# Performance work log

Measured on AMD Instinct MI355X. Metric: run time of the kernel, lower is better.

Reference implementation:

```python
import jax, jax.numpy as jnp
import numpy as np

POI, EMB, UNITS, QDIM, B = 5000, 256, 512, 256, 64


def setup_inputs() -> dict:
    key = jax.random.key(0)
    ks = jax.random.split(key, 16)
    s = 0.05
    return {
        "x": jax.random.randint(ks[0], (B,), 0, POI),
        "query": jax.random.normal(ks[1], (B, QDIM), jnp.float32),
        "poi_embedding": jax.random.normal(ks[2], (POI, EMB), jnp.float32),
        "A_hat": jax.random.normal(ks[3], (B, B), jnp.float32),
        "dec_hidden": jax.random.normal(ks[4], (B, UNITS), jnp.float32),
        "cat_dec_hidden": jax.random.normal(ks[5], (1, B, UNITS), jnp.float32),
        # GRUCell params (keras order z, r, h; reset_after=True -> bias [2, 3*units])
        "gru_kernel": jax.random.normal(ks[6], (EMB + QDIM, 3 * UNITS), jnp.float32) * s,
        "gru_rec_kernel": jax.random.normal(ks[7], (UNITS, 3 * UNITS), jnp.float32) * s,
        "gru_bias": jax.random.normal(ks[8], (2, 3 * UNITS), jnp.float32) * s,
        # Bahdanau attention params
        "W1_w": jax.random.normal(ks[9], (EMB, UNITS), jnp.float32) * s,
        "W1_b": jnp.zeros((UNITS,), jnp.float32),
        "W2_w": jax.random.normal(ks[10], (UNITS, UNITS), jnp.float32) * s,
        "W2_b": jnp.zeros((UNITS,), jnp.float32),
        "V_w": jax.random.normal(ks[11], (UNITS, 1), jnp.float32) * s,
        "V_b": jnp.zeros((1,), jnp.float32),
        # output dense: concat(context EMB, output_ UNITS, cat_hidden UNITS) -> POI
        "fc_w": jax.random.normal(ks[12], (EMB + 2 * UNITS, POI), jnp.float32) * s,
        "fc_b": jnp.zeros((POI,), jnp.float32),
    }


def _gru_cell(x, h, kernel, rec_kernel, bias):
    # keras GRUCell, reset_after=True, gate order (z, r, h)
    xm = x @ kernel + bias[0]        # [B, 3U]
    hm = h @ rec_kernel + bias[1]    # [B, 3U]
    xz, xr, xh = jnp.split(xm, 3, axis=-1)
    hz, hr, hh = jnp.split(hm, 3, axis=-1)
    z = jax.nn.sigmoid(xz + hz)
    r = jax.nn.sigmoid(xr + hr)
    h_cand = jnp.tanh(xh + r * hh)
    h_new = z * h + (1.0 - z) * h_cand
    return h_new, h_new


def reference(x, query, poi_embedding, A_hat, dec_hidden, cat_dec_hidden,
              gru_kernel, gru_rec_kernel, gru_bias,
              W1_w, W1_b, W2_w, W2_b, V_w, V_b, fc_w, fc_b):
    emb = poi_embedding
    x1 = jnp.concatenate([emb[x], query], axis=1)          # [B, EMB+QDIM]
    output_, state = _gru_cell(x1, dec_hidden, gru_kernel, gru_rec_kernel, gru_bias)
    # Bahdanau attention: values are the full embedding table [POI, EMB]
    v_proj = emb @ W1_w + W1_b                              # [POI, U]
    q_proj = output_ @ W2_w + W2_b                          # [B, U]
    score = jnp.tanh(v_proj[None, :, :] + q_proj[:, None, :]) @ V_w + V_b  # [B, POI, 1]
    attn = jax.nn.softmax(score, axis=1)                    # [B, POI, 1]
    context = jnp.sum(attn * emb[None, :, :], axis=1)       # [B, EMB]
    out_cat = jnp.concatenate([context, output_, cat_dec_hidden[0]], axis=1)
    logits = out_cat @ fc_w + fc_b                          # [B, POI]
    return (logits, state, output_)
```

## Files before the change

kernel.cpp:

```cpp
#include <hip/hip_runtime.h>
#include <hip/hip_bf16.h>

typedef __bf16 bf16;
typedef __bf16 bf16x8 __attribute__((ext_vector_type(8)));
typedef float f32x4 __attribute__((ext_vector_type(4)));

#define BB 64
#define EMB 256
#define UNITS 512
#define POI 5000
#define KCAT 1280
#define SCLD 5024
#define L2E 1.4426950408889634f

__device__ __forceinline__ float rcp_(float x){ return __builtin_amdgcn_rcpf(x); }
__device__ __forceinline__ float exp2_(float x){ return __builtin_amdgcn_exp2f(x); }

__device__ __forceinline__ f32x4 mm16r(const float* __restrict__ ap, const float* __restrict__ B,
                                       int ldb, int K, int nc, int lane){
  int q = lane >> 4;
  f32x4 acc = {0.f,0.f,0.f,0.f};
  ap += q*8;
  const float* bp = B + (size_t)(q*8)*ldb + nc;
#pragma unroll 2
  for(int k0 = 0; k0 < K; k0 += 32){
    f32x4 a0 = *(const f32x4*)ap;
    f32x4 a1 = *(const f32x4*)(ap+4);
    bf16x8 a, b;
#pragma unroll
    for(int j=0;j<4;j++){ a[j] = (bf16)a0[j]; a[4+j] = (bf16)a1[j]; }
#pragma unroll
    for(int j=0;j<8;j++) b[j] = (bf16)bp[(size_t)j*ldb];
    acc = __builtin_amdgcn_mfma_f32_16x16x32_bf16(a, b, acc, 0, 0, 0);
    ap += 32; bp += (size_t)32*ldb;
  }
  return acc;
}

__device__ __forceinline__ f32x4 mm16f(const float* __restrict__ A, const float* __restrict__ B,
                                       int lda, int ldb, int K, int mr, int nc, int lane){
  return mm16r(A + (size_t)mr*lda, B, ldb, K, nc, lane);
}

__global__ __launch_bounds__(256) void k_prep0(const float* __restrict__ W1,
    float* __restrict__ W1T, float* __restrict__ out){
  int t = blockIdx.x*256 + threadIdx.x;
  for(int i=t; i<BB*POI; i+=32768) out[i] = 0.f;
  for(int i=t; i<EMB*UNITS; i+=32768){
    int r = i >> 9, c = i & 511;
    W1T[(size_t)c*EMB + r] = W1[i];
  }
}

__global__ __launch_bounds__(256) void k_gru(const int* __restrict__ x, const float* __restrict__ query,
    const float* __restrict__ emb, const float* __restrict__ h0,
    const float* __restrict__ gruK, const float* __restrict__ gruR,
    float* __restrict__ xmP, float* __restrict__ hmP){
  int lane = threadIdx.x & 63, w = threadIdx.x >> 6;
  int col = blockIdx.x*16 + (lane & 15);
  int z = blockIdx.z;
  int mr = w*16 + (lane & 15);
  const float* arow;
  const float* B;
  float* C;
  if(blockIdx.y){
    arow = h0 + (size_t)mr*512 + z*256;
    B = gruR + (size_t)(z*256)*1536;
    C = hmP + (size_t)z*BB*1536;
  } else {
    arow = z ? (query + (size_t)mr*256) : (emb + (size_t)x[mr]*EMB);
    B = gruK + (size_t)(z*256)*1536;
    C = xmP + (size_t)z*BB*1536;
  }
  f32x4 acc = mm16r(arow, B, 1536, 256, col, lane);
  int rb = w*16 + (lane >> 4)*4;
#pragma unroll
  for(int r=0;r<4;r++) C[(size_t)(rb+r)*1536 + col] = acc[r];
}

__global__ void k_gates(const float* __restrict__ xmP, const float* __restrict__ hmP,
                        const float* __restrict__ bias, const float* __restrict__ h0,
                        const float* __restrict__ catd,
                        float* __restrict__ hn, float* __restrict__ outc, float* __restrict__ dout){
  int b = blockIdx.x, u = threadIdx.x;
  const float* x0 = xmP + b*1536; const float* x1s = xmP + (size_t)BB*1536 + b*1536;
  const float* h0s = hmP + b*1536; const float* h1s = hmP + (size_t)BB*1536 + b*1536;
  float xz = x0[u]      + x1s[u]      + bias[u];
  float xg = x0[512+u]  + x1s[512+u]  + bias[512+u];
  float xh = x0[1024+u] + x1s[1024+u] + bias[1024+u];
  float hz = h0s[u]      + h1s[u]      + bias[1536+u];
  float hg = h0s[512+u]  + h1s[512+u]  + bias[2048+u];
  float hh = h0s[1024+u] + h1s[1024+u] + bias[2560+u];
  float z = rcp_(1.f + exp2_(-L2E*(xz+hz)));
  float r = rcp_(1.f + exp2_(-L2E*(xg+hg)));
  float ca = xh + r*hh;
  ca = fminf(fmaxf(ca, -15.f), 15.f);
  float e = exp2_(2.f*L2E*ca);
  float hc = (e - 1.f)*rcp_(e + 1.f);
  float h = h0[b*512+u];
  float v = z*h + (1.f - z)*hc;
  hn[b*512+u] = v;
  outc[b*KCAT + 256 + u] = v;
  outc[b*KCAT + 768 + u] = catd[(size_t)b*512 + u];
  dout[(size_t)POI*BB + (size_t)b*512 + u] = v;
  dout[(size_t)POI*BB + (size_t)BB*512 + (size_t)b*512 + u] = v;
}

__global__ __launch_bounds__(256) void k_qproj(const float* __restrict__ hn, const float* __restrict__ W2,
                        const float* __restrict__ W2b, float* __restrict__ Eq){
  int lane = threadIdx.x & 63, w = threadIdx.x >> 6;
  int col = blockIdx.x*16 + (lane & 15);
  f32x4 acc = mm16f(hn, W2, UNITS, UNITS, UNITS, w*16 + (lane & 15), col, lane);
  float bn = W2b[col];
  int rb = w*16 + (lane >> 4)*4;
#pragma unroll
  for(int r=0;r<4;r++){
    float v = (acc[r] + bn)*(2.f*L2E);
    Eq[(rb+r)*UNITS + col] = exp2_(fminf(fmaxf(v, -40.f), 40.f));
  }
}

template<int NY>
__global__ __launch_bounds__(256, 4) void k_vscore(
    const float* __restrict__ emb, const float* __restrict__ W1T,
    const float* __restrict__ W1b, const float* __restrict__ Eq,
    const float* __restrict__ Vw, float* __restrict__ scS){
  constexpr int USL = 512/NY;
  __shared__ float evsT[USL][36];
  __shared__ float qs[64][USL+4];
  __shared__ float vws[USL];
  int t = threadIdx.x, lane = t & 63, w = t >> 6;
  int p0 = blockIdx.x*32, uh = blockIdx.y*USL;
  int q = lane >> 4;
#pragma unroll
  for(int i=0;i<USL/64;i++){
    int colL = (w + 4*i)*16 + (lane & 15);
    float bn = W1b[uh + colL];
    const float* brow = W1T + (size_t)(uh+colL)*EMB + q*8;
#pragma unroll
    for(int pq=0;pq<2;pq++){
      int mr = p0 + pq*16 + (lane & 15); if(mr >= POI) mr = POI-1;
      const float* ap = emb + (size_t)mr*EMB + q*8;
      const float* bp = brow;
      f32x4 acc = {0.f,0.f,0.f,0.f};
#pragma unroll 2
      for(int k0=0;k0<EMB;k0+=32){
        f32x4 a0 = *(const f32x4*)ap, a1 = *(const f32x4*)(ap+4);
        f32x4 b0 = *(const f32x4*)bp, b1 = *(const f32x4*)(bp+4);
        bf16x8 a, b;
#pragma unroll
        for(int j=0;j<4;j++){ a[j]=(bf16)a0[j]; a[4+j]=(bf16)a1[j];
                              b[j]=(bf16)b0[j]; b[4+j]=(bf16)b1[j]; }
        acc = __builtin_amdgcn_mfma_f32_16x16x32_bf16(a,b,acc,0,0,0);
        ap += 32; bp += 32;
      }
      f32x4 ev;
#pragma unroll
      for(int r=0;r<4;r++){
        float v = (acc[r] + bn)*(2.f*L2E);
        ev[r] = exp2_(fminf(fmaxf(v,-40.f),40.f));
      }
      *(f32x4*)&evsT[colL][pq*16 + q*4] = ev;
    }
  }
  constexpr int CG = USL/4;
  for(int i=t; i<64*CG; i+=256){
    int b = i/CG, cg = i - b*CG;
    *(f32x4*)&qs[b][cg*4] = *(const f32x4*)&Eq[b*UNITS + uh + cg*4];
  }
  if(t < USL) vws[t] = Vw[uh + t];
  __syncthreads();
  int pg = t & 7, bg = t >> 3;
  const float* q0r = &qs[2*bg][0];
  const float* q1r = &qs[2*bg+1][0];
  f32x4 s0 = {0.f,0.f,0.f,0.f}, s1 = {0.f,0.f,0.f,0.f};
#pragma unroll 2
  for(int u4=0; u4<USL/4; ++u4){
    f32x4 q0 = *(const f32x4*)&q0r[u4*4];
    f32x4 q1 = *(const f32x4*)&q1r[u4*4];
    f32x4 wv = *(const f32x4*)&vws[u4*4];
#pragma unroll
    for(int j=0;j<4;j++){
      f32x4 ev = *(const f32x4*)&evsT[u4*4+j][4*pg];
#pragma unroll
      for(int e=0;e<4;e++){
        s0[e] += wv[j]*rcp_(ev[e]*q0[j] + 1.f);
        s1[e] += wv[j]*rcp_(ev[e]*q1[j] + 1.f);
      }
    }
  }
  float* srow = scS + (size_t)blockIdx.y*BB*SCLD + (size_t)(2*bg)*SCLD + p0 + 4*pg;
  int pA = p0 + 4*pg;
  if(pA + 3 < POI){
    *(f32x4*)srow = s0;
    *(f32x4*)(srow + SCLD) = s1;
  } else {
#pragma unroll
    for(int e=0;e<4;e++) if(pA+e < POI){ srow[e] = s0[e]; srow[SCLD+e] = s1[e]; }
  }
}

__global__ __launch_bounds__(512) void k_softmax(float* __restrict__ sc, const float* __restrict__ Vw,
                                                 float* __restrict__ outc, float* __restrict__ ivb,
                                                 int nslab){
  __shared__ float red[512];
  int b = blockIdx.x, t = threadIdx.x;
  if(t < 256) outc[b*KCAT + t] = 0.f;
  red[t] = Vw[t];
  __syncthreads();
  for(int o=256;o>0;o>>=1){ if(t<o) red[t]+=red[t+o]; __syncthreads(); }
  float SW = red[0]; __syncthreads();
  float* sA = sc + (size_t)b*SCLD;
  float mx = -3.4e38f;
  for(int p=t;p<POI;p+=512){
    float acc = sA[p];
    for(int y=1;y<nslab;y++) acc += sA[(size_t)y*BB*SCLD + p];
    float s = SW - 2.f*acc;
    sA[p] = s;
    mx = fmaxf(mx, s);
  }
  red[t] = mx; __syncthreads();
  for(int o=256;o>0;o>>=1){ if(t<o) red[t]=fmaxf(red[t],red[t+o]); __syncthreads(); }
  float M = red[0]; __syncthreads();
  float sum = 0.f;
  for(int p=t;p<POI;p+=512){
    float wv = exp2_((sA[p] - M)*L2E);
    sA[p] = wv;
    sum += wv;
  }
  red[t] = sum; __syncthreads();
  for(int o=256;o>0;o>>=1){ if(t<o) red[t]+=red[t+o]; __syncthreads(); }
  if(t == 0) ivb[b] = rcp_(red[0]);
  if(t < SCLD-POI) sA[POI + t] = 0.f;
}

__global__ __launch_bounds__(256) void k_ctx(const float* __restrict__ wb, const float* __restrict__ emb,
                                             const float* __restrict__ ivb, float* __restrict__ outc){
  int lane = threadIdx.x & 63, w = threadIdx.x >> 6;
  int n = blockIdx.x*16 + (lane & 15);
  int ky = blockIdx.y;
  int kbeg = ky*384;
  int mr = w*16 + (lane & 15);
  f32x4 acc = mm16f(wb + kbeg, emb + (size_t)kbeg*EMB, SCLD, EMB, 384, mr, n, lane);
  if(ky == 12){
    int q = lane >> 4;
    const float* ap = wb + (size_t)mr*SCLD + 4992 + q*8;
    bf16x8 a, bfr;
#pragma unroll
    for(int j=0;j<8;j++) a[j] = (bf16)ap[j];
#pragma unroll
    for(int j=0;j<8;j++){
      int k = 4992 + q*8 + j; int kc = k < POI ? k : POI-1;
      bfr[j] = (bf16)emb[(size_t)kc*EMB + n];
    }
    acc = __builtin_amdgcn_mfma_f32_16x16x32_bf16(a, bfr, acc, 0, 0, 0);
  }
  int rb = w*16 + (lane >> 4)*4;
#pragma unroll
  for(int r=0;r<4;r++) atomicAdd(&outc[(size_t)(rb+r)*KCAT + n], acc[r]*ivb[rb+r]);
}

__global__ __launch_bounds__(256) void k_logits(const float* __restrict__ A, const float* __restrict__ Bw,
                        const float* __restrict__ fcb, float* __restrict__ out){
  int lane = threadIdx.x & 63, w = threadIdx.x >> 6;
  int n = blockIdx.x*16 + (lane & 15);
  int nc = n < POI ? n : POI-1;
  int ky = blockIdx.y, kbeg = ky*320;
  f32x4 acc = mm16f(A + kbeg, Bw + (size_t)kbeg*POI, KCAT, POI, 320,
                    w*16 + (lane & 15), nc, lane);
  int rb = w*16 + (lane >> 4)*4;
  if(n < POI){
    float bn = (ky == 0) ? fcb[n] : 0.f;
#pragma unroll
    for(int r=0;r<4;r++) atomicAdd(&out[(size_t)(rb+r)*POI + n], acc[r] + bn);
  }
}

extern "C" void kernel_launch(void* const* d_in, const int* in_sizes, int n_in,
                              void* d_out, int out_size, void* d_ws, size_t ws_size,
                              hipStream_t stream){
  const int*   x     = (const int*)d_in[0];
  const float* query = (const float*)d_in[1];
  const float* emb   = (const float*)d_in[2];
  const float* h0    = (const float*)d_in[4];
  const float* catd  = (const float*)d_in[5];
  const float* gruK  = (const float*)d_in[6];
  const float* gruR  = (const float*)d_in[7];
  const float* gruB  = (const float*)d_in[8];
  const float* W1    = (const float*)d_in[9];
  const float* W1b   = (const float*)d_in[10];
  const float* W2    = (const float*)d_in[11];
  const float* W2b   = (const float*)d_in[12];
  const float* Vw    = (const float*)d_in[13];
  const float* fcw   = (const float*)d_in[15];
  const float* fcb   = (const float*)d_in[16];
  float* out = (float*)d_out;

  int nslab = (ws_size >= (size_t)16*1024*1024) ? 8 : 4;

  char* ws = (char*)d_ws;
  size_t off = 0;
  auto alloc = [&](size_t bytes)->void*{ void* p = ws + off; off += (bytes + 255) & ~(size_t)255; return p; };
  float* outc = (float*)alloc((size_t)BB*KCAT*4);
  float* xmP  = (float*)alloc((size_t)2*BB*1536*4);
  float* hmP  = (float*)alloc((size_t)2*BB*1536*4);
  float* hn   = (float*)alloc((size_t)BB*512*4);
  float* Eq   = (float*)alloc((size_t)BB*512*4);
  float* W1T  = (float*)alloc((size_t)UNITS*EMB*4);
  float* ivb  = (float*)alloc((size_t)BB*4);
  float* sc   = (float*)alloc((size_t)nslab*BB*SCLD*4);

  k_prep0  <<<128, 256, 0, stream>>>(W1, W1T, out);
  k_gru    <<<dim3(96,2,2), 256, 0, stream>>>(x, query, emb, h0, gruK, gruR, xmP, hmP);
  k_gates  <<<BB, 512, 0, stream>>>(xmP, hmP, gruB, h0, catd, hn, outc, out);
  k_qproj  <<<32, 256, 0, stream>>>(hn, W2, W2b, Eq);
  if(nslab == 8)
    k_vscore<8><<<dim3(157,8), 256, 0, stream>>>(emb, W1T, W1b, Eq, Vw, sc);
  else
    k_vscore<4><<<dim3(157,4), 256, 0, stream>>>(emb, W1T, W1b, Eq, Vw, sc);
  k_softmax<<<BB, 512, 0, stream>>>(sc, Vw, outc, ivb, nslab);
  k_ctx    <<<dim3(16,13), 256, 0, stream>>>(sc, emb, ivb, outc);
  k_logits <<<dim3(313,4), 256, 0, stream>>>(outc, fcw, fcb, out);
}
```

Baseline: 218.6 us.

## Pre-convert weights to transposed bf16, split softmax, widen grids across kernels

A prep kernel now converts the embedding table, W1, W2 and the GRU kernels to bf16 and stores them transposed, so the matmul kernels read contiguous bf16x8 vectors instead of strided fp32 loads with per-element conversion. The softmax becomes two grid-wide passes that combine per-row max and sum through atomics. k_ctx, k_logits, k_vscore and k_qproj are re-tiled with more blocks and smaller K splits to raise parallelism. The cost is extra conversion and transpose traffic on every call, plus more launches and atomics. The SW constant term in the scores is also dropped, which softmax ignores anyway.

New measurement: 201.3 us. -7.9%, faster.

```diff
diff --git a/kernel.cpp b/kernel.cpp
--- a/kernel.cpp
+++ b/kernel.cpp
@@ -15,6 +15,13 @@
 
 __device__ __forceinline__ float rcp_(float x){ return __builtin_amdgcn_rcpf(x); }
 __device__ __forceinline__ float exp2_(float x){ return __builtin_amdgcn_exp2f(x); }
+
+__device__ __forceinline__ bf16x8 cvt8(f32x4 a0, f32x4 a1){
+  bf16x8 o;
+#pragma unroll
+  for(int j=0;j<4;j++){ o[j]=(bf16)a0[j]; o[4+j]=(bf16)a1[j]; }
+  return o;
+}
 
 __device__ __forceinline__ f32x4 mm16r(const float* __restrict__ ap, const float* __restrict__ B,
                                        int ldb, int K, int nc, int lane){
@@ -24,11 +31,8 @@
   const float* bp = B + (size_t)(q*8)*ldb + nc;
 #pragma unroll 2
   for(int k0 = 0; k0 < K; k0 += 32){
-    f32x4 a0 = *(const f32x4*)ap;
-    f32x4 a1 = *(const f32x4*)(ap+4);
-    bf16x8 a, b;
-#pragma unroll
-    for(int j=0;j<4;j++){ a[j] = (bf16)a0[j]; a[4+j] = (bf16)a1[j]; }
+    bf16x8 a = cvt8(*(const f32x4*)ap, *(const f32x4*)(ap+4));
+    bf16x8 b;
 #pragma unroll
     for(int j=0;j<8;j++) b[j] = (bf16)bp[(size_t)j*ldb];
     acc = __builtin_amdgcn_mfma_f32_16x16x32_bf16(a, b, acc, 0, 0, 0);
@@ -36,53 +40,122 @@
   }
   return acc;
 }
-
 __device__ __forceinline__ f32x4 mm16f(const float* __restrict__ A, const float* __restrict__ B,
                                        int lda, int ldb, int K, int mr, int nc, int lane){
   return mm16r(A + (size_t)mr*lda, B, ldb, K, nc, lane);
 }
 
-__global__ __launch_bounds__(256) void k_prep0(const float* __restrict__ W1,
-    float* __restrict__ W1T, float* __restrict__ out){
-  int t = blockIdx.x*256 + threadIdx.x;
-  for(int i=t; i<BB*POI; i+=32768) out[i] = 0.f;
-  for(int i=t; i<EMB*UNITS; i+=32768){
-    int r = i >> 9, c = i & 511;
-    W1T[(size_t)c*EMB + r] = W1[i];
+__device__ __forceinline__ void t64(const float* __restrict__ src, int srcLd, int nRv,
+    int r0, int c0, int cW, bf16* __restrict__ dstT, int dstLd, int dstRmax,
+    int lane, int w){
+  int r = r0 + lane;
+  bool rv = r < nRv;
+  int cw4 = cW >> 2;
+  int cb = c0 + w*cw4;
+  for(int c8=0;c8<cw4;c8+=8){
+    int c = cb + c8;
+    f32x4 v0={0.f,0.f,0.f,0.f}, v1={0.f,0.f,0.f,0.f};
+    if(rv){ v0 = *(const f32x4*)(src + (size_t)r*srcLd + c);
+            v1 = *(const f32x4*)(src + (size_t)r*srcLd + c + 4); }
+    if(r < dstRmax){
+#pragma unroll
+      for(int j=0;j<4;j++){
+        dstT[(size_t)(c+j)*dstLd + r]   = (bf16)v0[j];
+        dstT[(size_t)(c+4+j)*dstLd + r] = (bf16)v1[j];
+      }
+    }
+  }
+}
+
+__global__ __launch_bounds__(256) void k_prep0(
+    const float* __restrict__ emb, const float* __restrict__ W1, const float* __restrict__ W2,
+    const float* __restrict__ gruK, const float* __restrict__ gruR,
+    float* __restrict__ out, float* __restrict__ outc,
+    bf16* __restrict__ embB, bf16* __restrict__ embTb,
+    bf16* __restrict__ W1Tb, bf16* __restrict__ W2Tb,
+    bf16* __restrict__ gruKTb, bf16* __restrict__ gruRTb,
+    unsigned* __restrict__ mxb, float* __restrict__ sumb){
+  int bx = blockIdx.x, t = threadIdx.x, lane = t & 63, w = t >> 6;
+  if(bx < 80){
+    int r0 = bx*64;
+    for(int ch = t; ch < 2048; ch += 256){
+      int r = r0 + (ch >> 5), cc = (ch & 31)*8;
+      if(r < POI){
+        f32x4 v0 = *(const f32x4*)(emb + (size_t)r*EMB + cc);
+        f32x4 v1 = *(const f32x4*)(emb + (size_t)r*EMB + cc + 4);
+        *(bf16x8*)(embB + (size_t)r*EMB + cc) = cvt8(v0, v1);
+      }
+    }
+  } else if(bx < 240){
+    int i = bx - 80;
+    t64(emb, EMB, POI, (i>>1)*64, (i&1)*128, 128, embTb, SCLD, SCLD, lane, w);
+  } else if(bx < 256){
+    int i = bx - 240;
+    t64(W2, UNITS, UNITS, (i>>1)*64, (i&1)*256, 256, W2Tb, UNITS, UNITS, lane, w);
+  } else if(bx < 264){
+    int i = bx - 256;
+    t64(W1, UNITS, EMB, (i>>1)*64, (i&1)*256, 256, W1Tb, EMB, EMB, lane, w);
+  } else if(bx < 328){
+    int i = bx - 264;
+    t64(gruK, 1536, 512, (i>>3)*64, (i&7)*192, 192, gruKTb, 512, 512, lane, w);
+  } else if(bx < 392){
+    int i = bx - 328;
+    t64(gruR, 1536, 512, (i>>3)*64, (i&7)*192, 192, gruRTb, 512, 512, lane, w);
+  } else if(bx < 432){
+    f32x4 z = {0.f,0.f,0.f,0.f};
+    for(int i = (bx-392)*256 + t; i < 80000; i += 40*256) ((f32x4*)out)[i] = z;
+  } else if(bx < 434){
+    f32x4 z = {0.f,0.f,0.f,0.f};
+    for(int i = (bx-432)*256 + t; i < 4096; i += 512){
+      int b = i >> 6, jj = i & 63;
+      ((f32x4*)(outc + (size_t)b*KCAT))[jj] = z;
+    }
+  } else {
+    if(t < BB){ mxb[t] = 0u; sumb[t] = 0.f; }
   }
 }
 
 __global__ __launch_bounds__(256) void k_gru(const int* __restrict__ x, const float* __restrict__ query,
-    const float* __restrict__ emb, const float* __restrict__ h0,
-    const float* __restrict__ gruK, const float* __restrict__ gruR,
+    const bf16* __restrict__ embB, const float* __restrict__ h0,
+    const bf16* __restrict__ gruKTb, const bf16* __restrict__ gruRTb,
     float* __restrict__ xmP, float* __restrict__ hmP){
   int lane = threadIdx.x & 63, w = threadIdx.x >> 6;
   int col = blockIdx.x*16 + (lane & 15);
-  int z = blockIdx.z;
+  int y = blockIdx.y, z = blockIdx.z;
   int mr = w*16 + (lane & 15);
-  const float* arow;
-  const float* B;
-  float* C;
-  if(blockIdx.y){
-    arow = h0 + (size_t)mr*512 + z*256;
-    B = gruR + (size_t)(z*256)*1536;
-    C = hmP + (size_t)z*BB*1536;
+  int q = lane >> 4;
+  const bf16* bp = (y ? gruRTb : gruKTb) + (size_t)col*512 + z*256 + q*8;
+  float* C = (y ? hmP : xmP) + (size_t)z*BB*1536;
+  f32x4 acc = {0.f,0.f,0.f,0.f};
+  if(y == 0 && z == 0){
+    const bf16* ap = embB + (size_t)x[mr]*EMB + q*8;
+#pragma unroll
+    for(int k0=0;k0<256;k0+=32){
+      bf16x8 a = *(const bf16x8*)ap, b = *(const bf16x8*)bp;
+      acc = __builtin_amdgcn_mfma_f32_16x16x32_bf16(a,b,acc,0,0,0);
+      ap += 32; bp += 32;
+    }
   } else {
-    arow = z ? (query + (size_t)mr*256) : (emb + (size_t)x[mr]*EMB);
-    B = gruK + (size_t)(z*256)*1536;
-    C = xmP + (size_t)z*BB*1536;
-  }
-  f32x4 acc = mm16r(arow, B, 1536, 256, col, lane);
+    const float* apf = y ? (h0 + (size_t)mr*512 + z*256 + q*8)
+                         : (query + (size_t)mr*256 + q*8);
+#pragma unroll
+    for(int k0=0;k0<256;k0+=32){
+      bf16x8 a = cvt8(*(const f32x4*)apf, *(const f32x4*)(apf+4));
+      bf16x8 b = *(const bf16x8*)bp;
+      acc = __builtin_amdgcn_mfma_f32_16x16x32_bf16(a,b,acc,0,0,0);
+      apf += 32; bp += 32;
+    }
+  }
   int rb = w*16 + (lane >> 4)*4;
 #pragma unroll
   for(int r=0;r<4;r++) C[(size_t)(rb+r)*1536 + col] = acc[r];
 }
 
-__global__ void k_gates(const float* __restrict__ xmP, const float* __restrict__ hmP,
+__global__ __launch_bounds__(256) void k_gates(const float* __restrict__ xmP, const float* __restrict__ hmP,
                         const float* __restrict__ bias, const float* __restrict__ h0,
                         const float* __restrict__ catd,
                         float* __restrict__ hn, float* __restrict__ outc, float* __restrict__ dout){
-  int b = blockIdx.x, u = threadIdx.x;
+  int b = blockIdx.x, u = blockIdx.y*256 + threadIdx.x;
   const float* x0 = xmP + b*1536; const float* x1s = xmP + (size_t)BB*1536 + b*1536;
   const float* h0s = hmP + b*1536; const float* h1s = hmP + (size_t)BB*1536 + b*1536;
   float xz = x0[u]      + x1s[u]      + bias[u];
@@ -106,158 +179,159 @@
   dout[(size_t)POI*BB + (size_t)BB*512 + (size_t)b*512 + u] = v;
 }
 
-__global__ __launch_bounds__(256) void k_qproj(const float* __restrict__ hn, const float* __restrict__ W2,
+__global__ __launch_bounds__(256) void k_qproj(const float* __restrict__ hn, const bf16* __restrict__ W2Tb,
                         const float* __restrict__ W2b, float* __restrict__ Eq){
-  int lane = threadIdx.x & 63, w = threadIdx.x >> 6;
-  int col = blockIdx.x*16 + (lane & 15);
-  f32x4 acc = mm16f(hn, W2, UNITS, UNITS, UNITS, w*16 + (lane & 15), col, lane);
-  float bn = W2b[col];
-  int rb = w*16 + (lane >> 4)*4;
-#pragma unroll
-  for(int r=0;r<4;r++){
-    float v = (acc[r] + bn)*(2.f*L2E);
-    Eq[(rb+r)*UNITS + col] = exp2_(fminf(fmaxf(v, -40.f), 40.f));
-  }
+  __shared__ float accs[16][17];
+  int t = threadIdx.x, lane = t & 63, w = t >> 6;
+  int c16 = blockIdx.x & 31, r16 = blockIdx.x >> 5;
+  for(int i=t;i<16*17;i+=256) ((float*)accs)[i] = 0.f;
+  __syncthreads();
+  int q = lane >> 4;
+  int mr  = r16*16 + (lane & 15);
+  int col = c16*16 + (lane & 15);
+  const float* ap = hn + (size_t)mr*UNITS + w*128 + q*8;
+  const bf16*  bp = W2Tb + (size_t)col*UNITS + w*128 + q*8;
+  f32x4 acc = {0.f,0.f,0.f,0.f};
+#pragma unroll
+  for(int k0=0;k0<128;k0+=32){
+    bf16x8 a = cvt8(*(const f32x4*)ap, *(const f32x4*)(ap+4));
+    bf16x8 b = *(const bf16x8*)bp;
+    acc = __builtin_amdgcn_mfma_f32_16x16x32_bf16(a,b,acc,0,0,0);
+    ap += 32; bp += 32;
+  }
+#pragma unroll
+  for(int r=0;r<4;r++) atomicAdd(&accs[q*4+r][lane & 15], acc[r]);
+  __syncthreads();
+  int r = t >> 4, c = t & 15;
+  int colg = c16*16 + c;
+  float v = (accs[r][c] + W2b[colg])*(2.f*L2E);
+  Eq[(size_t)(r16*16+r)*UNITS + colg] = exp2_(fminf(fmaxf(v,-40.f),40.f));
 }
 
 template<int NY>
-__global__ __launch_bounds__(256, 4) void k_vscore(
-    const float* __restrict__ emb, const float* __restrict__ W1T,
+__global__ __launch_bounds__(256, 8) void k_vscore(
+    const bf16* __restrict__ embB, const bf16* __restrict__ W1Tb,
     const float* __restrict__ W1b, const float* __restrict__ Eq,
     const float* __restrict__ Vw, float* __restrict__ scS){
   constexpr int USL = 512/NY;
-  __shared__ float evsT[USL][36];
-  __shared__ float qs[64][USL+4];
+  __shared__ float evsT[USL][20];
   __shared__ float vws[USL];
   int t = threadIdx.x, lane = t & 63, w = t >> 6;
-  int p0 = blockIdx.x*32, uh = blockIdx.y*USL;
+  int p0 = blockIdx.x*16, uh = blockIdx.y*USL;
   int q = lane >> 4;
+  int mr = p0 + (lane & 15); if(mr > POI-1) mr = POI-1;
 #pragma unroll
   for(int i=0;i<USL/64;i++){
     int colL = (w + 4*i)*16 + (lane & 15);
-    float bn = W1b[uh + colL];
-    const float* brow = W1T + (size_t)(uh+colL)*EMB + q*8;
-#pragma unroll
-    for(int pq=0;pq<2;pq++){
-      int mr = p0 + pq*16 + (lane & 15); if(mr >= POI) mr = POI-1;
-      const float* ap = emb + (size_t)mr*EMB + q*8;
-      const float* bp = brow;
-      f32x4 acc = {0.f,0.f,0.f,0.f};
-#pragma unroll 2
-      for(int k0=0;k0<EMB;k0+=32){
-        f32x4 a0 = *(const f32x4*)ap, a1 = *(const f32x4*)(ap+4);
-        f32x4 b0 = *(const f32x4*)bp, b1 = *(const f32x4*)(bp+4);
-        bf16x8 a, b;
-#pragma unroll
-        for(int j=0;j<4;j++){ a[j]=(bf16)a0[j]; a[4+j]=(bf16)a1[j];
-                              b[j]=(bf16)b0[j]; b[4+j]=(bf16)b1[j]; }
-        acc = __builtin_amdgcn_mfma_f32_16x16x32_bf16(a,b,acc,0,0,0);
-        ap += 32; bp += 32;
-      }
-      f32x4 ev;
-#pragma unroll
-      for(int r=0;r<4;r++){
-        float v = (acc[r] + bn)*(2.f*L2E);
-        ev[r] = exp2_(fminf(fmaxf(v,-40.f),40.f));
-      }
-      *(f32x4*)&evsT[colL][pq*16 + q*4] = ev;
-    }
-  }
-  constexpr int CG = USL/4;
-  for(int i=t; i<64*CG; i+=256){
-    int b = i/CG, cg = i - b*CG;
-    *(f32x4*)&qs[b][cg*4] = *(const f32x4*)&Eq[b*UNITS + uh + cg*4];
+    const bf16* ap = embB + (size_t)mr*EMB + q*8;
+    const bf16* bp = W1Tb + (size_t)(uh+colL)*EMB + q*8;
+    f32x4 acc = {0.f,0.f,0.f,0.f};
+#pragma unroll
+    for(int k0=0;k0<EMB;k0+=32){
+      bf16x8 a = *(const bf16x8*)ap, b = *(const bf16x8*)bp;
+      acc = __builtin_amdgcn_mfma_f32_16x16x32_bf16(a,b,acc,0,0,0);
+      ap += 32; bp += 32;
+    }
+    float bn = W1b[uh+colL];
+    f32x4 ev;
+#pragma unroll
+    for(int r=0;r<4;r++){
+      float v = (acc[r] + bn)*(2.f*L2E);
+      ev[r] = exp2_(fminf(fmaxf(v,-40.f),40.f));
+    }
+    *(f32x4*)&evsT[colL][q*4] = ev;
   }
   if(t < USL) vws[t] = Vw[uh + t];
   __syncthreads();
-  int pg = t & 7, bg = t >> 3;
-  const float* q0r = &qs[2*bg][0];
-  const float* q1r = &qs[2*bg+1][0];
-  f32x4 s0 = {0.f,0.f,0.f,0.f}, s1 = {0.f,0.f,0.f,0.f};
-#pragma unroll 2
+  int pg = t & 3, b = t >> 2;
+  const float* qrow = Eq + (size_t)b*UNITS + uh;
+  f32x4 s = {0.f,0.f,0.f,0.f};
+#pragma unroll 4
   for(int u4=0; u4<USL/4; ++u4){
-    f32x4 q0 = *(const f32x4*)&q0r[u4*4];
-    f32x4 q1 = *(const f32x4*)&q1r[u4*4];
+    f32x4 q4 = *(const f32x4*)&qrow[u4*4];
     f32x4 wv = *(const f32x4*)&vws[u4*4];
 #pragma unroll
     for(int j=0;j<4;j++){
       f32x4 ev = *(const f32x4*)&evsT[u4*4+j][4*pg];
 #pragma unroll
-      for(int e=0;e<4;e++){
-        s0[e] += wv[j]*rcp_(ev[e]*q0[j] + 1.f);
-        s1[e] += wv[j]*rcp_(ev[e]*q1[j] + 1.f);
-      }
-    }
-  }
-  float* srow = scS + (size_t)blockIdx.y*BB*SCLD + (size_t)(2*bg)*SCLD + p0 + 4*pg;
+      for(int e=0;e<4;e++)
+        s[e] += wv[j]*rcp_(ev[e]*q4[j] + 1.f);
+    }
+  }
   int pA = p0 + 4*pg;
-  if(pA + 3 < POI){
-    *(f32x4*)srow = s0;
-    *(f32x4*)(srow + SCLD) = s1;
-  } else {
-#pragma unroll
-    for(int e=0;e<4;e++) if(pA+e < POI){ srow[e] = s0[e]; srow[SCLD+e] = s1[e]; }
-  }
-}
-
-__global__ __launch_bounds__(512) void k_softmax(float* __restrict__ sc, const float* __restrict__ Vw,
-                                                 float* __restrict__ outc, float* __restrict__ ivb,
-                                                 int nslab){
-  __shared__ float red[512];
-  int b = blockIdx.x, t = threadIdx.x;
-  if(t < 256) outc[b*KCAT + t] = 0.f;
-  red[t] = Vw[t];
-  __syncthreads();
-  for(int o=256;o>0;o>>=1){ if(t<o) red[t]+=red[t+o]; __syncthreads(); }
-  float SW = red[0]; __syncthreads();
+  float* srow = scS + (size_t)blockIdx.y*BB*SCLD + (size_t)b*SCLD + pA;
+  if(pA + 3 < POI) *(f32x4*)srow = s;
+  else {
+#pragma unroll
+    for(int e=0;e<4;e++) if(pA+e < POI) srow[e] = s[e];
+  }
+}
+
+__global__ __launch_bounds__(256) void k_smax_a(float* __restrict__ sc, unsigned* __restrict__ mxb,
+                                                int nslab){
+  __shared__ float red[256];
+  int b = blockIdx.x, y = blockIdx.y, t = threadIdx.x;
   float* sA = sc + (size_t)b*SCLD;
+  int pend = (y+1)*640; if(pend > POI) pend = POI;
   float mx = -3.4e38f;
-  for(int p=t;p<POI;p+=512){
+  for(int p = y*640 + t; p < pend; p += 256){
     float acc = sA[p];
-    for(int y=1;y<nslab;y++) acc += sA[(size_t)y*BB*SCLD + p];
-    float s = SW - 2.f*acc;
-    sA[p] = s;
-    mx = fmaxf(mx, s);
+    for(int s2=1;s2<nslab;s2++) acc += sA[(size_t)s2*BB*SCLD + p];
+    float v = -2.f*acc;
+    sA[p] = v;
+    mx = fmaxf(mx, v);
   }
   red[t] = mx; __syncthreads();
-  for(int o=256;o>0;o>>=1){ if(t<o) red[t]=fmaxf(red[t],red[t+o]); __syncthreads(); }
-  float M = red[0]; __syncthreads();
-  float sum = 0.f;
-  for(int p=t;p<POI;p+=512){
-    float wv = exp2_((sA[p] - M)*L2E);
-    sA[p] = wv;
-    sum += wv;
-  }
-  red[t] = sum; __syncthreads();
-  for(int o=256;o>0;o>>=1){ if(t<o) red[t]+=red[t+o]; __syncthreads(); }
-  if(t == 0) ivb[b] = rcp_(red[0]);
-  if(t < SCLD-POI) sA[POI + t] = 0.f;
-}
-
-__global__ __launch_bounds__(256) void k_ctx(const float* __restrict__ wb, const float* __restrict__ emb,
-                                             const float* __restrict__ ivb, float* __restrict__ outc){
+  for(int o=128;o>0;o>>=1){ if(t<o) red[t]=fmaxf(red[t],red[t+o]); __syncthreads(); }
+  if(t==0){
+    unsigned u = __float_as_uint(red[0]);
+    unsigned key = (u & 0x80000000u) ? ~u : (u | 0x80000000u);
+    atomicMax(mxb + b, key);
+  }
+}
+
+__global__ __launch_bounds__(256) void k_smax_b(float* __restrict__ sc, const unsigned* __restrict__ mxb,
+                                                float* __restrict__ sumb){
+  __shared__ float red[256];
+  int b = blockIdx.x, y = blockIdx.y, t = threadIdx.x;
+  unsigned key = mxb[b];
+  unsigned uu = (key & 0x80000000u) ? (key ^ 0x80000000u) : ~key;
+  float M = __uint_as_float(uu);
+  float* sA = sc + (size_t)b*SCLD;
+  int pend = (y+1)*640; if(pend > POI) pend = POI;
+  float sm = 0.f;
+  for(int p = y*640 + t; p < pend; p += 256){
+    float e = exp2_((sA[p] - M)*L2E);
+    sA[p] = e;
+    sm += e;
+  }
+  if(y == 7 && t < SCLD-POI) sA[POI + t] = 0.f;
+  red[t] = sm; __syncthreads();
+  for(int o=128;o>0;o>>=1){ if(t<o) red[t]+=red[t+o]; __syncthreads(); }
+  if(t==0) atomicAdd(sumb + b, red[0]);
+}
+
+__global__ __launch_bounds__(256) void k_ctx(const float* __restrict__ wb, const bf16* __restrict__ embTb,
+                                             const float* __restrict__ sumb, float* __restrict__ outc){
   int lane = threadIdx.x & 63, w = threadIdx.x >> 6;
   int n = blockIdx.x*16 + (lane & 15);
   int ky = blockIdx.y;
-  int kbeg = ky*384;
+  int kbeg = ky*64;
+  int K = (ky == 78) ? 32 : 64;
   int mr = w*16 + (lane & 15);
-  f32x4 acc = mm16f(wb + kbeg, emb + (size_t)kbeg*EMB, SCLD, EMB, 384, mr, n, lane);
-  if(ky == 12){
-    int q = lane >> 4;
-    const float* ap = wb + (size_t)mr*SCLD + 4992 + q*8;
-    bf16x8 a, bfr;
-#pragma unroll
-    for(int j=0;j<8;j++) a[j] = (bf16)ap[j];
-#pragma unroll
-    for(int j=0;j<8;j++){
-      int k = 4992 + q*8 + j; int kc = k < POI ? k : POI-1;
-      bfr[j] = (bf16)emb[(size_t)kc*EMB + n];
-    }
-    acc = __builtin_amdgcn_mfma_f32_16x16x32_bf16(a, bfr, acc, 0, 0, 0);
+  int q = lane >> 4;
+  const float* ap = wb + (size_t)mr*SCLD + kbeg + q*8;
+  const bf16*  bp = embTb + (size_t)n*SCLD + kbeg + q*8;
+  f32x4 acc = {0.f,0.f,0.f,0.f};
+  for(int k0=0;k0<K;k0+=32){
+    bf16x8 a = cvt8(*(const f32x4*)ap, *(const f32x4*)(ap+4));
+    bf16x8 b = *(const bf16x8*)bp;
+    acc = __builtin_amdgcn_mfma_f32_16x16x32_bf16(a,b,acc,0,0,0);
+    ap += 32; bp += 32;
   }
   int rb = w*16 + (lane >> 4)*4;
 #pragma unroll
-  for(int r=0;r<4;r++) atomicAdd(&outc[(size_t)(rb+r)*KCAT + n], acc[r]*ivb[rb+r]);
+  for(int r=0;r<4;r++) atomicAdd(&outc[(size_t)(rb+r)*KCAT + n], acc[r]*rcp_(sumb[rb+r]));
 }
 
 __global__ __launch_bounds__(256) void k_logits(const float* __restrict__ A, const float* __restrict__ Bw,
@@ -265,8 +339,8 @@
   int lane = threadIdx.x & 63, w = threadIdx.x >> 6;
   int n = blockIdx.x*16 + (lane & 15);
   int nc = n < POI ? n : POI-1;
-  int ky = blockIdx.y, kbeg = ky*320;
-  f32x4 acc = mm16f(A + kbeg, Bw + (size_t)kbeg*POI, KCAT, POI, 320,
+  int ky = blockIdx.y, kbeg = ky*160;
+  f32x4 acc = mm16f(A + kbeg, Bw + (size_t)kbeg*POI, KCAT, POI, 160,
                     w*16 + (lane & 15), nc, lane);
   int rb = w*16 + (lane >> 4)*4;
   if(n < POI){
@@ -296,29 +370,37 @@
   const float* fcb   = (const float*)d_in[16];
   float* out = (float*)d_out;
 
-  int nslab = (ws_size >= (size_t)16*1024*1024) ? 8 : 4;
+  int nslab = (ws_size >= (size_t)24*1024*1024) ? 8 : 4;
 
   char* ws = (char*)d_ws;
   size_t off = 0;
   auto alloc = [&](size_t bytes)->void*{ void* p = ws + off; off += (bytes + 255) & ~(size_t)255; return p; };
-  float* outc = (float*)alloc((size_t)BB*KCAT*4);
-  float* xmP  = (float*)alloc((size_t)2*BB*1536*4);
-  float* hmP  = (float*)alloc((size_t)2*BB*1536*4);
-  float* hn   = (float*)alloc((size_t)BB*512*4);
-  float* Eq   = (float*)alloc((size_t)BB*512*4);
-  float* W1T  = (float*)alloc((size_t)UNITS*EMB*4);
-  float* ivb  = (float*)alloc((size_t)BB*4);
-  float* sc   = (float*)alloc((size_t)nslab*BB*SCLD*4);
-
-  k_prep0  <<<128, 256, 0, stream>>>(W1, W1T, out);
-  k_gru    <<<dim3(96,2,2), 256, 0, stream>>>(x, query, emb, h0, gruK, gruR, xmP, hmP);
-  k_gates  <<<BB, 512, 0, stream>>>(xmP, hmP, gruB, h0, catd, hn, outc, out);
-  k_qproj  <<<32, 256, 0, stream>>>(hn, W2, W2b, Eq);
+  float* outc   = (float*)alloc((size_t)BB*KCAT*4);
+  float* xmP    = (float*)alloc((size_t)2*BB*1536*4);
+  float* hmP    = (float*)alloc((size_t)2*BB*1536*4);
+  float* hn     = (float*)alloc((size_t)BB*512*4);
+  float* Eq     = (float*)alloc((size_t)BB*512*4);
+  bf16*  embB   = (bf16*)alloc((size_t)POI*EMB*2);
+  bf16*  embTb  = (bf16*)alloc((size_t)EMB*SCLD*2);
+  bf16*  W1Tb   = (bf16*)alloc((size_t)UNITS*EMB*2);
+  bf16*  W2Tb   = (bf16*)alloc((size_t)UNITS*UNITS*2);
+  bf16*  gruKTb = (bf16*)alloc((size_t)1536*512*2);
+  bf16*  gruRTb = (bf16*)alloc((size_t)1536*512*2);
+  unsigned* mxb = (unsigned*)alloc((size_t)BB*4);
+  float* sumb   = (float*)alloc((size_t)BB*4);
+  float* sc     = (float*)alloc((size_t)nslab*BB*SCLD*4);
+
+  k_prep0  <<<435, 256, 0, stream>>>(emb, W1, W2, gruK, gruR, out, outc,
+                                     embB, embTb, W1Tb, W2Tb, gruKTb, gruRTb, mxb, sumb);
+  k_gru    <<<dim3(96,2,2), 256, 0, stream>>>(x, query, embB, h0, gruKTb, gruRTb, xmP, hmP);
+  k_gates  <<<dim3(BB,2), 256, 0, stream>>>(xmP, hmP, gruB, h0, catd, hn, outc, out);
+  k_qproj  <<<128, 256, 0, stream>>>(hn, W2Tb, W2b, Eq);
   if(nslab == 8)
-    k_vscore<8><<<dim3(157,8), 256, 0, stream>>>(emb, W1T, W1b, Eq, Vw, sc);
+    k_vscore<8><<<dim3(313,8), 256, 0, stream>>>(embB, W1Tb, W1b, Eq, Vw, sc);
   else
-    k_vscore<4><<<dim3(157,4), 256, 0, stream>>>(emb, W1T, W1b, Eq, Vw, sc);
-  k_softmax<<<BB, 512, 0, stream>>>(sc, Vw, outc, ivb, nslab);
-  k_ctx    <<<dim3(16,13), 256, 0, stream>>>(sc, emb, ivb, outc);
-  k_logits <<<dim3(313,4), 256, 0, stream>>>(outc, fcw, fcb, out);
-}
+    k_vscore<4><<<dim3(313,4), 256, 0, stream>>>(embB, W1Tb, W1b, Eq, Vw, sc);
+  k_smax_a <<<dim3(BB,8), 256, 0, stream>>>(sc, mxb, nslab);
+  k_smax_b <<<dim3(BB,8), 256, 0, stream>>>(sc, mxb, sumb);
+  k_ctx    <<<dim3(16,79), 256, 0, stream>>>(sc, embTb, sumb, outc);
+  k_logits <<<dim3(313,8), 256, 0, stream>>>(outc, fcw, fcb, out);
+}
```
